# Performance work log

Hardware: AMD Instinct MI355X
Metric: run time of the kernel (lower is better)

Reference implementation:

```python
import jax, jax.numpy as jnp
import numpy as np

V, D, H, L, S_MAX = 32000, 1024, 16, 4, 1024
HD = D // H          # head dim = 64
FF = 4 * D           # mlp hidden = 4096
B, S = 2, 1024


def _layernorm(x, w, b, eps=1e-5):
    mu = jnp.mean(x, axis=-1, keepdims=True)
    var = jnp.mean(jnp.square(x - mu), axis=-1, keepdims=True)
    return (x - mu) * jax.lax.rsqrt(var + eps) * w + b


def setup_inputs() -> dict:
    key = jax.random.key(0)
    ks = jax.random.split(key, 16)
    r = lambda k, shape: (jax.random.normal(k, shape, dtype=jnp.float32) * 0.02)
    return {
        "input_ids": jax.random.randint(ks[0], (B, S), 0, V),
        "tok_emb": r(ks[1], (V, D)),
        "pos_emb": r(ks[2], (S_MAX, D)),
        "ln1_w": jnp.ones((L, D)), "ln1_b": jnp.zeros((L, D)),
        "ln2_w": jnp.ones((L, D)), "ln2_b": jnp.zeros((L, D)),
        "q_w": r(ks[3], (L, D, D)), "q_b": jnp.zeros((L, D)),
        "k_w": r(ks[4], (L, D, D)), "k_b": jnp.zeros((L, D)),
        "v_w": r(ks[5], (L, D, D)), "v_b": jnp.zeros((L, D)),
        "o_w": r(ks[6], (L, D, D)), "o_b": jnp.zeros((L, D)),
        "fc1_w": r(ks[7], (L, FF, D)), "fc1_b": jnp.zeros((L, FF)),
        "fc2_w": r(ks[8], (L, D, FF)), "fc2_b": jnp.zeros((L, D)),
        "lnf_w": jnp.ones((D,)), "lnf_b": jnp.zeros((D,)),
        "head_w": r(ks[9], (V, D)),
    }


def reference(input_ids, tok_emb, pos_emb, ln1_w, ln1_b, ln2_w, ln2_b,
              q_w, q_b, k_w, k_b, v_w, v_b, o_w, o_b,
              fc1_w, fc1_b, fc2_w, fc2_b, lnf_w, lnf_b, head_w):
    b, s = input_ids.shape
    x = tok_emb[input_ids] + pos_emb[:s][None, :, :]          # [B,S,D]
    causal = jnp.tril(jnp.ones((s, s), dtype=bool))           # [S,S]
    scale = 1.0 / np.sqrt(HD)
    for i in range(L):
        # --- causal MHA block ---
        h = _layernorm(x, ln1_w[i], ln1_b[i])
        q = (h @ q_w[i].T + q_b[i]).reshape(b, s, H, HD)
        k = (h @ k_w[i].T + k_b[i]).reshape(b, s, H, HD)
        v = (h @ v_w[i].T + v_b[i]).reshape(b, s, H, HD)
        scores = jnp.einsum('bqhd,bkhd->bhqk', q, k) * scale  # [B,H,S,S]
        scores = jnp.where(causal[None, None], scores, -jnp.inf)
        attn = jax.nn.softmax(scores, axis=-1)
        y = jnp.einsum('bhqk,bkhd->bqhd', attn, v).reshape(b, s, D)
        x = x + (y @ o_w[i].T + o_b[i])
        # --- GELU MLP block (exact gelu, matching torch F.gelu default) ---
        h = _layernorm(x, ln2_w[i], ln2_b[i])
        h = jax.nn.gelu(h @ fc1_w[i].T + fc1_b[i], approximate=False)
        x = x + (h @ fc2_w[i].T + fc2_b[i])
    x = _layernorm(x, lnf_w, lnf_b)
    logits = x[:, -1, :] @ head_w.T                           # [B,V]
    return logits
```

## Files before the change

### kernel.cpp

```cpp
#include <hip/hip_runtime.h>

#define V_SIZE 32000
#define D_DIM  1024
#define H_HEADS 16
#define L_LAYERS 4
#define HD_DIM 64
#define FF_DIM 4096
#define B_BATCH 2
#define S_SEQ  1024
#define M_ROWS (B_BATCH*S_SEQ)
#define KSPL   2

typedef short  s16x8 __attribute__((ext_vector_type(8)));
typedef unsigned short u16x8 __attribute__((ext_vector_type(8)));
typedef float  f32x4 __attribute__((ext_vector_type(4)));
typedef unsigned short u16;
typedef unsigned int   u32;

__device__ inline u16 f2bf(float f){
    u32 u = __float_as_uint(f);
    return (u16)((u + 0x7FFFu + ((u >> 16) & 1u)) >> 16);
}
__device__ inline float b2f(u32 v){ return __uint_as_float(v << 16); }

__device__ inline float gelu_f(float v){
    float y = 0.7978845608f * (v + 0.044715f*v*v*v);
    y = fmaxf(-15.f, fminf(15.f, y));
    float u = __expf(-2.f*y);
    return v / (1.f + u);
}

__device__ inline char* lds_swz(void* base, int row, int byteoff){
    return (char*)base + row*128 + (byteoff ^ ((row & 7) << 4));
}

__device__ inline void gload16(const u16* g, u16* l){
    __builtin_amdgcn_global_load_lds(
        (const __attribute__((address_space(1))) void*)g,
        (__attribute__((address_space(3))) void*)l, 16, 0, 0);
}

__device__ inline int swz_src_col(int lin){
    int row = lin >> 3, s8 = lin & 7;
    return (s8*8) ^ ((row & 7) << 3);
}

__device__ inline s16x8 cvt8(float4 a, float4 b){
    s16x8 o;
    o[0]=(short)f2bf(a.x); o[1]=(short)f2bf(a.y);
    o[2]=(short)f2bf(a.z); o[3]=(short)f2bf(a.w);
    o[4]=(short)f2bf(b.x); o[5]=(short)f2bf(b.y);
    o[6]=(short)f2bf(b.z); o[7]=(short)f2bf(b.w);
    return o;
}

__global__ __launch_bounds__(256) void cvt_all_k(
    const float* __restrict__ qw, const float* __restrict__ kw,
    const float* __restrict__ vw, const float* __restrict__ ow,
    const float* __restrict__ f1w, const float* __restrict__ f2w,
    u16* __restrict__ w_qkv, u16* __restrict__ w_o,
    u16* __restrict__ w_f1, u16* __restrict__ w_f2)
{
    const long M1 = 1L << 20;
    const int bx = blockIdx.x;
    const float* s; u16* d; long base;
    if (bx < 3072){
        int which = bx >> 10;
        s = (which==0) ? qw : ((which==1) ? kw : vw);
        base = (long)(bx & 1023) * 4096;
        long layer = base >> 20, rem = base & (M1 - 1);
        d = w_qkv + layer*3*M1 + which*M1 + rem;
        s += base;
    } else if (bx < 4096){
        base = (long)(bx - 3072) * 4096; s = ow  + base; d = w_o  + base;
    } else if (bx < 8192){
        base = (long)(bx - 4096) * 4096; s = f1w + base; d = w_f1 + base;
    } else {
        base = (long)(bx - 8192) * 4096; s = f2w + base; d = w_f2 + base;
    }
    const int t8 = threadIdx.x * 8;
#pragma unroll
    for (int j = 0; j < 2; j++){
        const float* sp = s + j*2048 + t8;
        float4 v0 = *(const float4*)(sp);
        float4 v1 = *(const float4*)(sp + 4);
        *(s16x8*)(d + j*2048 + t8) = cvt8(v0, v1);
    }
}

__global__ __launch_bounds__(256) void embed_ln_k(
    const int* __restrict__ ids, const float* __restrict__ tok,
    const float* __restrict__ pos, const float* __restrict__ lw,
    const float* __restrict__ lb, float* __restrict__ x, u16* __restrict__ h)
{
    int row = blockIdx.x;
    int id  = ids[row];
    int s   = row & (S_SEQ - 1);
    int t   = threadIdx.x;
    float4 tv = *(const float4*)(tok + (size_t)id * D_DIM + t*4);
    float4 pv = *(const float4*)(pos + (size_t)s  * D_DIM + t*4);
    float4 vv;
    vv.x = tv.x + pv.x; vv.y = tv.y + pv.y; vv.z = tv.z + pv.z; vv.w = tv.w + pv.w;
    *(float4*)(x + (size_t)row * D_DIM + t*4) = vv;
    float sm  = vv.x + vv.y + vv.z + vv.w;
    float ss = vv.x*vv.x + vv.y*vv.y + vv.z*vv.z + vv.w*vv.w;
#pragma unroll
    for (int off = 1; off < 64; off <<= 1){
        sm += __shfl_xor(sm, off);
        ss += __shfl_xor(ss, off);
    }
    __shared__ float red[8];
    const int wid = t >> 6, lane = t & 63;
    if (lane == 0){ red[wid] = sm; red[4 + wid] = ss; }
    __syncthreads();
    sm = red[0] + red[1] + red[2] + red[3];
    ss = red[4] + red[5] + red[6] + red[7];
    float mu   = sm * (1.0f/1024.0f);
    float rstd = rsqrtf(ss * (1.0f/1024.0f) - mu*mu + 1e-5f);
    float4 wv = *(const float4*)(lw + t*4);
    float4 bv = *(const float4*)(lb + t*4);
    uint2 pk;
    pk.x = (u32)f2bf((vv.x-mu)*rstd*wv.x + bv.x) | ((u32)f2bf((vv.y-mu)*rstd*wv.y + bv.y) << 16);
    pk.y = (u32)f2bf((vv.z-mu)*rstd*wv.z + bv.z) | ((u32)f2bf((vv.w-mu)*rstd*wv.w + bv.w) << 16);
    *(uint2*)(h + (size_t)row * D_DIM + t*4) = pk;
}

__global__ __launch_bounds__(256) void reduce_ln_k(
    const u16* __restrict__ part, const float* __restrict__ bias,
    float* __restrict__ x,
    const float* __restrict__ lw, const float* __restrict__ lb,
    u16* __restrict__ h)
{
    const int row = blockIdx.x, t = threadIdx.x;
    const size_t off = (size_t)row * D_DIM + t*4;
    float4 a = *(float4*)(x + off);
    float4 bv = *(const float4*)(bias + t*4);
    a.x += bv.x; a.y += bv.y; a.z += bv.z; a.w += bv.w;
#pragma unroll
    for (int si = 0; si < KSPL; si++){
        uint2 pv = *(const uint2*)(part + (size_t)si * M_ROWS * D_DIM + off);
        a.x += b2f(pv.x & 0xffffu); a.y += b2f(pv.x >> 16);
        a.z += b2f(pv.y & 0xffffu); a.w += b2f(pv.y >> 16);
    }
    *(float4*)(x + off) = a;
    float sm = a.x + a.y + a.z + a.w;
    float ss = a.x*a.x + a.y*a.y + a.z*a.z + a.w*a.w;
#pragma unroll
    for (int o2 = 1; o2 < 64; o2 <<= 1){
        sm += __shfl_xor(sm, o2);
        ss += __shfl_xor(ss, o2);
    }
    __shared__ float red[8];
    const int wid = t >> 6, lane = t & 63;
    if (lane == 0){ red[wid] = sm; red[4 + wid] = ss; }
    __syncthreads();
    sm = red[0] + red[1] + red[2] + red[3];
    ss = red[4] + red[5] + red[6] + red[7];
    float mu   = sm * (1.0f/1024.0f);
    float rstd = rsqrtf(ss * (1.0f/1024.0f) - mu*mu + 1e-5f);
    float4 wv = *(const float4*)(lw + t*4);
    float4 lbv = *(const float4*)(lb + t*4);
    uint2 pk;
    pk.x = (u32)f2bf((a.x-mu)*rstd*wv.x + lbv.x) | ((u32)f2bf((a.y-mu)*rstd*wv.y + lbv.y) << 16);
    pk.y = (u32)f2bf((a.z-mu)*rstd*wv.z + lbv.z) | ((u32)f2bf((a.w-mu)*rstd*wv.w + lbv.w) << 16);
    *(uint2*)(h + (size_t)row * D_DIM + t*4) = pk;
}

__global__ __launch_bounds__(256) void gemm_fc1_k(
    const u16* __restrict__ A, const u16* __restrict__ Bw,
    const float* __restrict__ b0, u16* __restrict__ outB, int Ndim, int Kdim)
{
    const int nx = gridDim.x, ny = gridDim.y;
    const int nwg = nx*ny;
    int orig = blockIdx.y*nx + blockIdx.x;
    int wg = (orig & 7)*(nwg >> 3) + (orig >> 3);
    const int bm = wg % nx;
    const int bn = wg / nx;

    const int nk = Kdim >> 6;

    __shared__ __align__(16) u16 As[2][128*64];
    __shared__ __align__(16) u16 Bs[2][128*64];

    const int t = threadIdx.x;
    const int wid = t >> 6, lane = t & 63, lr = lane & 15, lg = lane >> 4;
    const int wr = wid >> 1, wc = wid & 1;

    f32x4 acc[4][4];
#pragma unroll
    for (int m=0;m<4;m++)
#pragma unroll
        for (int n=0;n<4;n++) acc[m][n] = (f32x4){0.f,0.f,0.f,0.f};

    const u16* Abase = A  + (size_t)(bm*128)*Kdim;
    const u16* Bbase = Bw + (size_t)(bn*128)*Kdim;

    auto stage = [&](int koff, int buf){
#pragma unroll
        for (int i=0;i<4;i++){
            int lin = i*256 + t;
            int row = lin >> 3;
            int sc  = swz_src_col(lin);
            gload16(Abase + (size_t)row*Kdim + koff + sc, &As[buf][lin*8]);
        }
#pragma unroll
        for (int i=0;i<4;i++){
            int lin = i*256 + t;
            int row = lin >> 3;
            int sc  = swz_src_col(lin);
            gload16(Bbase + (size_t)row*Kdim + koff + sc, &Bs[buf][lin*8]);
        }
    };

    stage(0, 0);
    __syncthreads();
    int cb = 0;
    for (int ki = 0; ki < nk; ki++){
        if (ki+1 < nk) stage((ki+1)*64, cb^1);
#pragma unroll
        for (int kk=0;kk<2;kk++){
            s16x8 a[4], b[4];
#pragma unroll
            for (int m=0;m<4;m++)
                a[m] = *(s16x8*)lds_swz(As[cb], wr*64 + m*16 + lr, kk*64 + lg*16);
#pragma unroll
            for (int n=0;n<4;n++)
                b[n] = *(s16x8*)lds_swz(Bs[cb], wc*64 + n*16 + lr, kk*64 + lg*16);
#pragma unroll
            for (int m=0;m<4;m++)
#pragma unroll
                for (int n=0;n<4;n++)
                    acc[m][n] = __builtin_amdgcn_mfma_f32_16x16x32_bf16(a[m], b[n], acc[m][n], 0, 0, 0);
        }
        __syncthreads();
        cb ^= 1;
    }

#pragma unroll
    for (int n=0;n<4;n++){
        int col = bn*128 + wc*64 + n*16 + lr;
        float bvv = b0[col];
#pragma unroll
        for (int m=0;m<4;m++){
            int row0 = bm*128 + wr*64 + m*16 + lg*4;
#pragma unroll
            for (int j=0;j<4;j++){
                int row = row0 + j;
                float val = gelu_f(acc[m][n][j] + bvv);
                outB[(size_t)row * Ndim + col] = f2bf(val);
            }
        }
    }
}

template<int QSEG>
__global__ __launch_bounds__(256) void gemm64o_k(
    const u16* __restrict__ A, const u16* __restrict__ Bw,
    const float* __restrict__ b0, const float* __restrict__ b1, const float* __restrict__ b2,
    u16* __restrict__ outB, int Ndim, int Kdim)
{
    const int nx = gridDim.x, ny = gridDim.y;
    const int nwg = nx*ny;
    int orig = blockIdx.y*nx + blockIdx.x;
    int wg = (orig & 7)*(nwg >> 3) + (orig >> 3);
    const int bm = wg % nx;
    const int bn = wg / nx;
    const int nk = Kdim >> 6;

    __shared__ __align__(16) u16 As[2][64*64];
    __shared__ __align__(16) u16 Bs[2][128*64];

    const int t = threadIdx.x;
    const int wid = t >> 6, lane = t & 63, lr = lane & 15, lg = lane >> 4;
    const int wr = wid >> 1, wc = wid & 1;

    f32x4 acc[2][4];
#pragma unroll
    for (int m=0;m<2;m++)
#pragma unroll
        for (int n=0;n<4;n++) acc[m][n] = (f32x4){0.f,0.f,0.f,0.f};

    const u16* Abase = A  + (size_t)(bm*64)*Kdim;
    const u16* Bbase = Bw + (size_t)(bn*128)*Kdim;

    auto stage = [&](int koff, int buf){
#pragma unroll
        for (int i=0;i<2;i++){
            int lin = i*256 + t;
            int row = lin >> 3;
            int sc  = swz_src_col(lin);
            gload16(Abase + (size_t)row*Kdim + koff + sc, &As[buf][lin*8]);
        }
#pragma unroll
        for (int i=0;i<4;i++){
            int lin = i*256 + t;
            int row = lin >> 3;
            int sc  = swz_src_col(lin);
            gload16(Bbase + (size_t)row*Kdim + koff + sc, &Bs[buf][lin*8]);
        }
    };

    stage(0, 0);
    __syncthreads();
    int cb = 0;
    for (int ki = 0; ki < nk; ki++){
        if (ki+1 < nk) stage((ki+1)*64, cb^1);
#pragma unroll
        for (int kk=0;kk<2;kk++){
            s16x8 a[2], b[4];
#pragma unroll
            for (int m=0;m<2;m++)
                a[m] = *(s16x8*)lds_swz(As[cb], wr*32 + m*16 + lr, kk*64 + lg*16);
#pragma unroll
            for (int n=0;n<4;n++)
                b[n] = *(s16x8*)lds_swz(Bs[cb], wc*64 + n*16 + lr, kk*64 + lg*16);
#pragma unroll
            for (int m=0;m<2;m++)
#pragma unroll
                for (int n=0;n<4;n++)
                    acc[m][n] = __builtin_amdgcn_mfma_f32_16x16x32_bf16(a[m], b[n], acc[m][n], 0, 0, 0);
        }
        __syncthreads();
        cb ^= 1;
    }

#pragma unroll
    for (int n=0;n<4;n++){
        int col = bn*128 + wc*64 + n*16 + lr;
        int which = col >> 10;
        const float* bp = (which==0) ? b0 : ((which==1) ? b1 : b2);
        float bvv = bp[col & 1023];
        float scl = (which == QSEG) ? 0.125f : 1.0f;
#pragma unroll
        for (int m=0;m<2;m++){
            int row0 = bm*64 + wr*32 + m*16 + lg*4;
#pragma unroll
            for (int j=0;j<4;j++){
                int row = row0 + j;
                float val = (acc[m][n][j] + bvv) * scl;
                outB[(size_t)row * Ndim + col] = f2bf(val);
            }
        }
    }
}

__global__ __launch_bounds__(256) void gemm64_k(
    const u16* __restrict__ A, const u16* __restrict__ Bw,
    u16* __restrict__ outP, int Ndim, int Kdim, int kper)
{
    const int nx = gridDim.x, ny = gridDim.y;
    const int nwg = nx*ny*gridDim.z;
    int orig = (blockIdx.z*ny + blockIdx.y)*nx + blockIdx.x;
    int wg = (orig & 7)*(nwg >> 3) + (orig >> 3);
    const int bm = wg % nx; wg /= nx;
    const int bn = wg % ny;
    const int z  = wg / ny;
    const int kbeg = z * kper;
    const int nk = kper >> 6;

    __shared__ __align__(16) u16 As[2][64*64];
    __shared__ __align__(16) u16 Bs[2][128*64];

    const int t = threadIdx.x;
    const int wid = t >> 6, lane = t & 63, lr = lane & 15, lg = lane >> 4;
    const int wr = wid >> 1, wc = wid & 1;

    f32x4 acc[2][4];
#pragma unroll
    for (int m=0;m<2;m++)
#pragma unroll
        for (int n=0;n<4;n++) acc[m][n] = (f32x4){0.f,0.f,0.f,0.f};

    const u16* Abase = A  + (size_t)(bm*64)*Kdim + kbeg;
    const u16* Bbase = Bw + (size_t)(bn*128)*Kdim + kbeg;

    auto stage = [&](int koff, int buf){
#pragma unroll
        for (int i=0;i<2;i++){
            int lin = i*256 + t;
            int row = lin >> 3;
            int sc  = swz_src_col(lin);
            gload16(Abase + (size_t)row*Kdim + koff + sc, &As[buf][lin*8]);
        }
#pragma unroll
        for (int i=0;i<4;i++){
            int lin = i*256 + t;
            int row = lin >> 3;
            int sc  = swz_src_col(lin);
            gload16(Bbase + (size_t)row*Kdim + koff + sc, &Bs[buf][lin*8]);
        }
    };

    stage(0, 0);
    __syncthreads();
    int cb = 0;
    for (int ki = 0; ki < nk; ki++){
        if (ki+1 < nk) stage((ki+1)*64, cb^1);
#pragma unroll
        for (int kk=0;kk<2;kk++){
            s16x8 a[2], b[4];
#pragma unroll
            for (int m=0;m<2;m++)
                a[m] = *(s16x8*)lds_swz(As[cb], wr*32 + m*16 + lr, kk*64 + lg*16);
#pragma unroll
            for (int n=0;n<4;n++)
                b[n] = *(s16x8*)lds_swz(Bs[cb], wc*64 + n*16 + lr, kk*64 + lg*16);
#pragma unroll
            for (int m=0;m<2;m++)
#pragma unroll
                for (int n=0;n<4;n++)
                    acc[m][n] = __builtin_amdgcn_mfma_f32_16x16x32_bf16(a[m], b[n], acc[m][n], 0, 0, 0);
        }
        __syncthreads();
        cb ^= 1;
    }

#pragma unroll
    for (int n=0;n<4;n++){
        int col = bn*128 + wc*64 + n*16 + lr;
#pragma unroll
        for (int m=0;m<2;m++){
            int row0 = bm*64 + wr*32 + m*16 + lg*4;
#pragma unroll
            for (int j=0;j<4;j++){
                int row = row0 + j;
                outP[(size_t)z * M_ROWS * Ndim + (size_t)row * Ndim + col] = f2bf(acc[m][n][j]);
            }
        }
    }
}

__global__ __launch_bounds__(256) void attn_k(
    const u16* __restrict__ qkv, u16* __restrict__ y)
{
    const int gx = gridDim.x;
    const int nwg = gx * gridDim.y;
    int orig = blockIdx.y*gx + blockIdx.x;
    int wg = (orig & 7)*(nwg >> 3) + (orig >> 3);
    const int p  = wg % gx;
    const int bh = wg / gx;
    const int b  = bh >> 4, h = bh & 15;

    const int s_lo = p, s_hi = 15 - p;
    const int ntiles = s_hi + 1;

    __shared__ __align__(16) u16 Ks[2][64*64];
    __shared__ __align__(16) u16 VTs[2][64*64];
    __shared__ __align__(16) u16 Ps[4][16*64];

    const int t = threadIdx.x, wid = t >> 6, lane = t & 63, lr = lane & 15, lg = lane >> 4;
    const size_t rowb = (size_t)b * S_SEQ;
    const u16* qp = qkv + h*HD_DIM;
    const u16* kp = qkv + 1024 + h*HD_DIM;
    const u16* vp = qkv + 2048 + h*HD_DIM;

    const int qw_lo = s_lo*64 + wid*16;
    const int qw_hi = s_hi*64 + wid*16;

    s16x8 aq_lo[2], aq_hi[2];
#pragma unroll
    for (int kc=0;kc<2;kc++){
        aq_lo[kc] = *(const s16x8*)(qp + (rowb + qw_lo + lr) * 3072 + kc*32 + lg*8);
        aq_hi[kc] = *(const s16x8*)(qp + (rowb + qw_hi + lr) * 3072 + kc*32 + lg*8);
    }

    f32x4 o_lo[4], o_hi[4];
#pragma unroll
    for (int n=0;n<4;n++){ o_lo[n] = (f32x4){0.f,0.f,0.f,0.f}; o_hi[n] = (f32x4){0.f,0.f,0.f,0.f}; }
    float l_lo[4] = {0.f,0.f,0.f,0.f}, l_hi[4] = {0.f,0.f,0.f,0.f};

    const int kpr = t >> 3, dsl = t & 7;
    u16x8 vr0, vr1;

    auto issueK = [&](int kt, int buf){
#pragma unroll
        for (int i=0;i<2;i++){
            int lin = i*256 + t;
            int row = lin >> 3;
            int sc  = swz_src_col(lin);
            gload16(kp + (rowb + kt*64 + row)*3072 + sc, &Ks[buf][lin*8]);
        }
    };
    auto loadV = [&](int kt){
        vr0 = *(const u16x8*)(vp + (rowb + kt*64 + 2*kpr    )*3072 + dsl*8);
        vr1 = *(const u16x8*)(vp + (rowb + kt*64 + 2*kpr + 1)*3072 + dsl*8);
    };
    auto writeVT = [&](int buf){
#pragma unroll
        for (int j=0;j<8;j++){
            u32 pk = (u32)vr0[j] | ((u32)vr1[j] << 16);
            *(u32*)lds_swz(VTs[buf], dsl*8 + j, kpr*4) = pk;
        }
    };

    auto doStrip = [&](const s16x8* aq, f32x4* o, float* lsum, int qwS, int kt, bool diag, int cb){
        f32x4 sf[4];
#pragma unroll
        for (int n=0;n<4;n++) sf[n] = (f32x4){0.f,0.f,0.f,0.f};
        __builtin_amdgcn_s_setprio(1);
#pragma unroll
        for (int kc=0;kc<2;kc++){
#pragma unroll
            for (int n=0;n<4;n++){
                s16x8 bk = *(s16x8*)lds_swz(Ks[cb], n*16 + lr, kc*64 + lg*16);
                sf[n] = __builtin_amdgcn_mfma_f32_16x16x32_bf16(aq[kc], bk, sf[n], 0, 0, 0);
            }
        }
        __builtin_amdgcn_s_setprio(0);
        float rs[4] = {0.f,0.f,0.f,0.f};
#pragma unroll
        for (int n=0;n<4;n++){
            int key = kt*64 + n*16 + lr;
#pragma unroll
            for (int j=0;j<4;j++){
                float pe = __expf(sf[n][j]);
                if (diag && key > qwS + lg*4 + j) pe = 0.f;
                sf[n][j] = pe; rs[j] += pe;
            }
        }
#pragma unroll
        for (int off=1; off<16; off<<=1){
#pragma unroll
            for (int j=0;j<4;j++) rs[j] += __shfl_xor(rs[j], off);
        }
#pragma unroll
        for (int j=0;j<4;j++) lsum[j] += rs[j];
        u16* Pw = Ps[wid];
#pragma unroll
        for (int n=0;n<4;n++)
#pragma unroll
            for (int j=0;j<4;j++)
                *(u16*)lds_swz(Pw, lg*4 + j, (n*16 + lr)*2) = f2bf(sf[n][j]);
        __builtin_amdgcn_s_setprio(1);
#pragma unroll
        for (int kc=0;kc<2;kc++){
            s16x8 pa = *(s16x8*)lds_swz(Pw, lr, kc*64 + lg*16);
#pragma unroll
            for (int n=0;n<4;n++){
                s16x8 bv = *(s16x8*)lds_swz(VTs[cb], n*16 + lr, kc*64 + lg*16);
                o[n] = __builtin_amdgcn_mfma_f32_16x16x32_bf16(pa, bv, o[n], 0, 0, 0);
            }
        }
        __builtin_amdgcn_s_setprio(0);
    };

    issueK(0, 0); loadV(0); writeVT(0);
    __syncthreads();
    int cb = 0;
    for (int kt = 0; kt < ntiles; kt++){
        const bool more = (kt+1 < ntiles);
        if (more){ issueK(kt+1, cb^1); loadV(kt+1); }

        doStrip(aq_hi, o_hi, l_hi, qw_hi, kt, kt == s_hi, cb);
        if (kt <= s_lo)
            doStrip(aq_lo, o_lo, l_lo, qw_lo, kt, kt == s_lo, cb);

        if (more) writeVT(cb^1);
        __syncthreads();
        cb ^= 1;
    }

    float inv_lo[4], inv_hi[4];
#pragma unroll
    for (int j=0;j<4;j++){ inv_lo[j] = 1.0f / l_lo[j]; inv_hi[j] = 1.0f / l_hi[j]; }
#pragma unroll
    for (int n=0;n<4;n++)
#pragma unroll
        for (int j=0;j<4;j++){
            y[(rowb + qw_hi + lg*4 + j) * D_DIM + h*HD_DIM + n*16 + lr] = f2bf(o_hi[n][j] * inv_hi[j]);
            y[(rowb + qw_lo + lg*4 + j) * D_DIM + h*HD_DIM + n*16 + lr] = f2bf(o_lo[n][j] * inv_lo[j]);
        }
}

__global__ __launch_bounds__(256) void attn_last_k(
    const u16* __restrict__ q2, const u16* __restrict__ kv,
    float* __restrict__ Yp, float* __restrict__ psp)
{
    const int chunk = blockIdx.x;
    const int bh = blockIdx.y;
    const int b = bh >> 4, h = bh & 15;
    const int t = threadIdx.x;
    const size_t rowb = (size_t)b * S_SEQ;
    __shared__ float qs[64];
    __shared__ float ps[256];
    __shared__ float red[4];
    __shared__ float yred[4][64];
    if (t < 64) qs[t] = b2f(q2[b*1024 + h*HD_DIM + t]);
    __syncthreads();
    int k = chunk*256 + t;
    const u16* krow = kv + (rowb + k)*2048 + h*HD_DIM;
    float s = 0.f;
#pragma unroll
    for (int j=0;j<8;j++){
        u16x8 kv8 = *(const u16x8*)(krow + j*8);
#pragma unroll
        for (int e=0;e<8;e++) s += qs[j*8+e] * b2f((u32)(unsigned short)kv8[e]);
    }
    float p = __expf(s);
    ps[t] = p;
    float sp_ = p;
#pragma unroll
    for (int off=1; off<64; off<<=1) sp_ += __shfl_xor(sp_, off);
    if ((t & 63) == 0) red[t>>6] = sp_;
    __syncthreads();
    if (t == 0) psp[chunk*32 + bh] = red[0]+red[1]+red[2]+red[3];
    int d = t & 63, c = t >> 6;
    float acc = 0.f;
    const u16* vbase = kv + (rowb + chunk*256 + c*64)*2048 + 1024 + h*HD_DIM + d;
    for (int kk=0; kk<64; kk++)
        acc += ps[c*64 + kk] * b2f((u32)vbase[(size_t)kk*2048]);
    yred[c][d] = acc;
    __syncthreads();
    if (t < 64)
        Yp[(chunk*32 + bh)*64 + t] = yred[0][t]+yred[1][t]+yred[2][t]+yred[3][t];
}

template<int MODE>
__global__ __launch_bounds__(256) void rowpair_k(
    const u16* __restrict__ A0, const u16* __restrict__ A1,
    const float* __restrict__ Yp, const float* __restrict__ psp,
    const float* __restrict__ x2in,
    const float* __restrict__ lw, const float* __restrict__ lb,
    const u16* __restrict__ W, const float* __restrict__ bias,
    const float* __restrict__ xresid,
    float* __restrict__ outF, u16* __restrict__ outB,
    int Ndim, int Kdim)
{
    __shared__ u16 As16[2][1024];
    __shared__ float red[8];
    const int t = threadIdx.x, wid = t >> 6, lane = t & 63;

    if (MODE == 0){
        for (int idx = t; idx < 2048; idx += 256){
            int r = idx >> 10, d10 = idx & 1023;
            int bh = r*16 + (d10 >> 6), d = d10 & 63;
            float psum = psp[bh] + psp[32+bh] + psp[64+bh] + psp[96+bh];
            float yv = Yp[bh*64+d] + Yp[(32+bh)*64+d] + Yp[(64+bh)*64+d] + Yp[(96+bh)*64+d];
            As16[r][d10] = f2bf(yv / psum);
        }
        __syncthreads();
    }
    if (MODE == 1){
#pragma unroll
        for (int r = 0; r < 2; r++){
            float4 vv = *(const float4*)(x2in + r*1024 + t*4);
            float sm = vv.x + vv.y + vv.z + vv.w;
            float ss = vv.x*vv.x + vv.y*vv.y + vv.z*vv.z + vv.w*vv.w;
#pragma unroll
            for (int o2 = 1; o2 < 64; o2 <<= 1){
                sm += __shfl_xor(sm, o2);
                ss += __shfl_xor(ss, o2);
            }
            if (lane == 0){ red[wid] = sm; red[4+wid] = ss; }
            __syncthreads();
            sm = red[0]+red[1]+red[2]+red[3];
            ss = red[4]+red[5]+red[6]+red[7];
            float mu = sm * (1.0f/1024.0f);
            float rstd = rsqrtf(ss * (1.0f/1024.0f) - mu*mu + 1e-5f);
            float4 wv  = *(const float4*)(lw + t*4);
            float4 lbv = *(const float4*)(lb + t*4);
            As16[r][t*4+0] = f2bf((vv.x-mu)*rstd*wv.x + lbv.x);
            As16[r][t*4+1] = f2bf((vv.y-mu)*rstd*wv.y + lbv.y);
            As16[r][t*4+2] = f2bf((vv.z-mu)*rstd*wv.z + lbv.z);
            As16[r][t*4+3] = f2bf((vv.w-mu)*rstd*wv.w + lbv.w);
            __syncthreads();
        }
    }

    const u16* pa0 = (MODE==0 || MODE==1) ? (const u16*)As16[0] : A0;
    const u16* pa1 = (MODE==0 || MODE==1) ? (const u16*)As16[1] : A1;

    const int colsPerBlock = Ndim >> 8;
    const int colsPerWave  = colsPerBlock >> 2;
    const int nj = Kdim >> 9;
    for (int cc = 0; cc < colsPerWave; cc++){
        int col = blockIdx.x * colsPerBlock + wid * colsPerWave + cc;
        const u16* wrow = W + (size_t)col * Kdim;
        float s0 = 0.f, s1 = 0.f;
        for (int j = 0; j < nj; j++){
            int k = j*512 + lane*8;
            u16x8 wv = *(const u16x8*)(wrow + k);
            u16x8 a0 = *(const u16x8*)(pa0 + k);
            u16x8 a1 = *(const u16x8*)(pa1 + k);
#pragma unroll
            for (int e=0;e<8;e++){
                float wf = b2f((u32)wv[e]);
                s0 += b2f((u32)a0[e]) * wf;
                s1 += b2f((u32)a1[e]) * wf;
            }
        }
#pragma unroll
        for (int off=1; off<64; off<<=1){
            s0 += __shfl_xor(s0, off);
            s1 += __shfl_xor(s1, off);
        }
        if (lane == 0){
            float bv = bias[col];
            if (MODE == 0){
                outF[col]         = xresid[(size_t)(S_SEQ-1)*D_DIM + col]   + bv + s0;
                outF[D_DIM + col] = xresid[(size_t)(2*S_SEQ-1)*D_DIM + col] + bv + s1;
            } else if (MODE == 1){
                outB[col]         = f2bf(gelu_f(s0 + bv));
                outB[Ndim + col]  = f2bf(gelu_f(s1 + bv));
            } else if (MODE == 2){
                outF[col]         = x2in[col]         + bv + s0;
                outF[D_DIM + col] = x2in[D_DIM + col] + bv + s1;
            } else {
                outB[col]         = f2bf((s0 + bv) * 0.125f);
                outB[Ndim + col]  = f2bf((s1 + bv) * 0.125f);
            }
        }
    }
}

__global__ __launch_bounds__(256) void head_ln_k(
    const float* __restrict__ x3, const float* __restrict__ w, const float* __restrict__ bb,
    const float* __restrict__ hw, float* __restrict__ out)
{
    __shared__ float xs[2*D_DIM];
    __shared__ float red[8];
    int t = threadIdx.x, wid = t >> 6, lane = t & 63;
#pragma unroll
    for (int r = 0; r < 2; r++){
        float4 vv = *(const float4*)(x3 + r*D_DIM + t*4);
        float s  = vv.x + vv.y + vv.z + vv.w;
        float ss = vv.x*vv.x + vv.y*vv.y + vv.z*vv.z + vv.w*vv.w;
#pragma unroll
        for (int off = 1; off < 64; off <<= 1){
            s  += __shfl_xor(s,  off);
            ss += __shfl_xor(ss, off);
        }
        if (lane == 0){ red[wid] = s; red[4+wid] = ss; }
        __syncthreads();
        s  = red[0]+red[1]+red[2]+red[3];
        ss = red[4]+red[5]+red[6]+red[7];
        float mu   = s * (1.0f/1024.0f);
        float rstd = rsqrtf(ss * (1.0f/1024.0f) - mu*mu + 1e-5f);
        float4 wv = *(const float4*)(w  + t*4);
        float4 bv = *(const float4*)(bb + t*4);
        xs[r*D_DIM + t*4+0] = (vv.x-mu)*rstd*wv.x + bv.x;
        xs[r*D_DIM + t*4+1] = (vv.y-mu)*rstd*wv.y + bv.y;
        xs[r*D_DIM + t*4+2] = (vv.z-mu)*rstd*wv.z + bv.z;
        xs[r*D_DIM + t*4+3] = (vv.w-mu)*rstd*wv.w + bv.w;
        __syncthreads();
    }
    int vrow = blockIdx.x * 4 + wid;
    float s0 = 0.f, s1 = 0.f;
#pragma unroll
    for (int it=0; it<4; it++){
        int j = it*64 + lane;
        float4 w4 = *(const float4*)(hw + (size_t)vrow * D_DIM + j*4);
        float4 x0 = *(const float4*)&xs[j*4];
        float4 x1 = *(const float4*)&xs[D_DIM + j*4];
        s0 += w4.x*x0.x + w4.y*x0.y + w4.z*x0.z + w4.w*x0.w;
        s1 += w4.x*x1.x + w4.y*x1.y + w4.z*x1.z + w4.w*x1.w;
    }
#pragma unroll
    for (int off=1; off<64; off<<=1){
        s0 += __shfl_xor(s0, off);
        s1 += __shfl_xor(s1, off);
    }
    if (lane == 0){
        out[vrow]          = s0;
        out[V_SIZE + vrow] = s1;
    }
}

extern "C" void kernel_launch(void* const* d_in, const int* in_sizes, int n_in,
                              void* d_out, int out_size, void* d_ws, size_t ws_size,
                              hipStream_t stream)
{
    (void)in_sizes; (void)n_in; (void)out_size; (void)ws_size;
    const int*   ids  = (const int*)  d_in[0];
    const float* tok  = (const float*)d_in[1];
    const float* pos  = (const float*)d_in[2];
    const float* ln1w = (const float*)d_in[3];
    const float* ln1b = (const float*)d_in[4];
    const float* ln2w = (const float*)d_in[5];
    const float* ln2b = (const float*)d_in[6];
    const float* qw   = (const float*)d_in[7];
    const float* qbi  = (const float*)d_in[8];
    const float* kw   = (const float*)d_in[9];
    const float* kbi  = (const float*)d_in[10];
    const float* vw   = (const float*)d_in[11];
    const float* vbi  = (const float*)d_in[12];
    const float* ow   = (const float*)d_in[13];
    const float* obi  = (const float*)d_in[14];
    const float* f1w  = (const float*)d_in[15];
    const float* f1b  = (const float*)d_in[16];
    const float* f2w  = (const float*)d_in[17];
    const float* f2b  = (const float*)d_in[18];
    const float* lnfw = (const float*)d_in[19];
    const float* lnfb = (const float*)d_in[20];
    const float* hw   = (const float*)d_in[21];

    const long MD = (long)1024*1024;
    char* p = (char*)d_ws;
    float* x    = (float*)p; p += (size_t)M_ROWS * D_DIM * 4;
    u16* h      = (u16*)p;   p += (size_t)M_ROWS * D_DIM * 2;
    u16* qkvbuf = (u16*)p;   p += (size_t)M_ROWS * 3072 * 2;
    u16* ybuf   = (u16*)p;   p += (size_t)M_ROWS * D_DIM * 2;
    u16* h1     = (u16*)p;   p += (size_t)M_ROWS * FF_DIM * 2;
    u16* part   = (u16*)p;   p += (size_t)KSPL * M_ROWS * D_DIM * 2;
    u16* wbuf   = (u16*)p;   p += (size_t)48 * MD * 2;
    u16*   q2   = (u16*)p;   p += 2 * D_DIM * 2;
    float* x2   = (float*)p; p += 2 * D_DIM * 4;
    float* x3   = (float*)p; p += 2 * D_DIM * 4;
    u16*   g2   = (u16*)p;   p += 2 * FF_DIM * 2;
    float* Yp   = (float*)p; p += 4 * 32 * 64 * 4;
    float* psp  = (float*)p; p += 4 * 32 * 4;
    float* logits = (float*)d_out;

    u16* w_qkv = wbuf;
    u16* w_o   = wbuf + 12*MD;
    u16* w_f1  = wbuf + 16*MD;
    u16* w_f2  = wbuf + 32*MD;

    cvt_all_k<<<dim3(12288), 256, 0, stream>>>(
        qw, kw, vw, ow, f1w, f2w, w_qkv, w_o, w_f1, w_f2);

    embed_ln_k<<<dim3(M_ROWS), 256, 0, stream>>>(ids, tok, pos, ln1w, ln1b, x, h);

    for (int i = 0; i < L_LAYERS - 1; i++){
        gemm64o_k<0><<<dim3(32, 24), 256, 0, stream>>>(
            h, w_qkv + (size_t)i*3*MD,
            qbi + i*D_DIM, kbi + i*D_DIM, vbi + i*D_DIM,
            qkvbuf, 3072, D_DIM);
        attn_k<<<dim3(8, 32), 256, 0, stream>>>(qkvbuf, ybuf);
        gemm64_k<<<dim3(32, 8, KSPL), 256, 0, stream>>>(
            ybuf, w_o + (size_t)i*MD, part, D_DIM, D_DIM, D_DIM/KSPL);
        reduce_ln_k<<<dim3(M_ROWS), 256, 0, stream>>>(
            part, obi + i*D_DIM, x, ln2w + i*D_DIM, ln2b + i*D_DIM, h);
        gemm_fc1_k<<<dim3(16, 32), 256, 0, stream>>>(
            h, w_f1 + (size_t)i*4*MD, f1b + i*FF_DIM, h1, FF_DIM, D_DIM);
        gemm64_k<<<dim3(32, 8, KSPL), 256, 0, stream>>>(
            h1, w_f2 + (size_t)i*4*MD, part, D_DIM, FF_DIM, FF_DIM/KSPL);
        reduce_ln_k<<<dim3(M_ROWS), 256, 0, stream>>>(
            part, f2b + i*D_DIM, x, ln1w + (i+1)*D_DIM, ln1b + (i+1)*D_DIM, h);
    }

    const int L3 = L_LAYERS - 1;
    gemm64o_k<-1><<<dim3(32, 16), 256, 0, stream>>>(
        h, w_qkv + (size_t)L3*3*MD + MD,
        kbi + L3*D_DIM, vbi + L3*D_DIM, vbi + L3*D_DIM,
        qkvbuf, 2048, D_DIM);
    rowpair_k<3><<<dim3(256), 256, 0, stream>>>(
        h + (size_t)(S_SEQ-1)*D_DIM, h + (size_t)(2*S_SEQ-1)*D_DIM,
        nullptr, nullptr, nullptr, nullptr, nullptr,
        w_qkv + (size_t)L3*3*MD, qbi + L3*D_DIM, nullptr,
        nullptr, q2, D_DIM, D_DIM);
    attn_last_k<<<dim3(4, 32), 256, 0, stream>>>(q2, qkvbuf, Yp, psp);
    rowpair_k<0><<<dim3(256), 256, 0, stream>>>(
        nullptr, nullptr, Yp, psp, nullptr, nullptr, nullptr,
        w_o + (size_t)L3*MD, obi + L3*D_DIM, x,
        x2, nullptr, D_DIM, D_DIM);
    rowpair_k<1><<<dim3(256), 256, 0, stream>>>(
        nullptr, nullptr, nullptr, nullptr, x2,
        ln2w + L3*D_DIM, ln2b + L3*D_DIM,
        w_f1 + (size_t)L3*4*MD, f1b + L3*FF_DIM, nullptr,
        nullptr, g2, FF_DIM, D_DIM);
    rowpair_k<2><<<dim3(256), 256, 0, stream>>>(
        g2, g2 + FF_DIM, nullptr, nullptr, x2, nullptr, nullptr,
        w_f2 + (size_t)L3*4*MD, f2b + L3*D_DIM, nullptr,
        x3, nullptr, D_DIM, FF_DIM);
    head_ln_k<<<dim3(V_SIZE/4), 256, 0, stream>>>(x3, lnfw, lnfb, hw, logits);
}
```

Before: 538.9 us.

## Split attention lo/hi query strips across 8 waves in 512-thread blocks

Doubles the attention block to 512 threads so four waves handle the low query strip and four handle the high strip, instead of each wave processing both strips serially. K loads are done by the upper half of threads and V transpose by the lower half. This raises per-block parallelism and halves per-wave register state, but the waves on the low strip sit idle once past their diagonal tile, so work is imbalanced inside the block and barrier waits grow.

```diff
diff --git a/kernel.cpp b/kernel.cpp
--- a/kernel.cpp
+++ b/kernel.cpp
@@ -430,7 +430,7 @@
     }
 }
 
-__global__ __launch_bounds__(256) void attn_k(
+__global__ __launch_bounds__(512) void attn_k(
     const u16* __restrict__ qkv, u16* __restrict__ y)
 {
     const int gx = gridDim.x;
@@ -446,7 +446,7 @@
 
     __shared__ __align__(16) u16 Ks[2][64*64];
     __shared__ __align__(16) u16 VTs[2][64*64];
-    __shared__ __align__(16) u16 Ps[4][16*64];
+    __shared__ __align__(16) u16 Ps[8][16*64];
 
     const int t = threadIdx.x, wid = t >> 6, lane = t & 63, lr = lane & 15, lg = lane >> 4;
     const size_t rowb = (size_t)b * S_SEQ;
@@ -454,46 +454,51 @@
     const u16* kp = qkv + 1024 + h*HD_DIM;
     const u16* vp = qkv + 2048 + h*HD_DIM;
 
-    const int qw_lo = s_lo*64 + wid*16;
-    const int qw_hi = s_hi*64 + wid*16;
-
-    s16x8 aq_lo[2], aq_hi[2];
-#pragma unroll
-    for (int kc=0;kc<2;kc++){
-        aq_lo[kc] = *(const s16x8*)(qp + (rowb + qw_lo + lr) * 3072 + kc*32 + lg*8);
-        aq_hi[kc] = *(const s16x8*)(qp + (rowb + qw_hi + lr) * 3072 + kc*32 + lg*8);
-    }
-
-    f32x4 o_lo[4], o_hi[4];
-#pragma unroll
-    for (int n=0;n<4;n++){ o_lo[n] = (f32x4){0.f,0.f,0.f,0.f}; o_hi[n] = (f32x4){0.f,0.f,0.f,0.f}; }
-    float l_lo[4] = {0.f,0.f,0.f,0.f}, l_hi[4] = {0.f,0.f,0.f,0.f};
+    const int s  = (wid >= 4) ? s_hi : s_lo;
+    const int wq = wid & 3;
+    const int qw = s*64 + wq*16;
+
+    s16x8 aq[2];
+#pragma unroll
+    for (int kc=0;kc<2;kc++)
+        aq[kc] = *(const s16x8*)(qp + (rowb + qw + lr) * 3072 + kc*32 + lg*8);
+
+    f32x4 o[4];
+#pragma unroll
+    for (int n=0;n<4;n++) o[n] = (f32x4){0.f,0.f,0.f,0.f};
+    float lsum[4] = {0.f,0.f,0.f,0.f};
 
     const int kpr = t >> 3, dsl = t & 7;
     u16x8 vr0, vr1;
 
     auto issueK = [&](int kt, int buf){
-#pragma unroll
-        for (int i=0;i<2;i++){
-            int lin = i*256 + t;
-            int row = lin >> 3;
-            int sc  = swz_src_col(lin);
-            gload16(kp + (rowb + kt*64 + row)*3072 + sc, &Ks[buf][lin*8]);
+        if (t >= 256){
+#pragma unroll
+            for (int i=0;i<2;i++){
+                int lin = i*256 + (t - 256);
+                int row = lin >> 3;
+                int sc  = swz_src_col(lin);
+                gload16(kp + (rowb + kt*64 + row)*3072 + sc, &Ks[buf][lin*8]);
+            }
         }
     };
     auto loadV = [&](int kt){
-        vr0 = *(const u16x8*)(vp + (rowb + kt*64 + 2*kpr    )*3072 + dsl*8);
-        vr1 = *(const u16x8*)(vp + (rowb + kt*64 + 2*kpr + 1)*3072 + dsl*8);
+        if (t < 256){
+            vr0 = *(const u16x8*)(vp + (rowb + kt*64 + 2*kpr    )*3072 + dsl*8);
+            vr1 = *(const u16x8*)(vp + (rowb + kt*64 + 2*kpr + 1)*3072 + dsl*8);
+        }
     };
     auto writeVT = [&](int buf){
-#pragma unroll
-        for (int j=0;j<8;j++){
-            u32 pk = (u32)vr0[j] | ((u32)vr1[j] << 16);
-            *(u32*)lds_swz(VTs[buf], dsl*8 + j, kpr*4) = pk;
+        if (t < 256){
+#pragma unroll
+            for (int j=0;j<8;j++){
+                u32 pk = (u32)vr0[j] | ((u32)vr1[j] << 16);
+                *(u32*)lds_swz(VTs[buf], dsl*8 + j, kpr*4) = pk;
+            }
         }
     };
 
-    auto doStrip = [&](const s16x8* aq, f32x4* o, float* lsum, int qwS, int kt, bool diag, int cb){
+    auto doTile = [&](int kt, int cb){
         f32x4 sf[4];
 #pragma unroll
         for (int n=0;n<4;n++) sf[n] = (f32x4){0.f,0.f,0.f,0.f};
@@ -507,6 +512,7 @@
             }
         }
         __builtin_amdgcn_s_setprio(0);
+        const bool diag = (kt == s);
         float rs[4] = {0.f,0.f,0.f,0.f};
 #pragma unroll
         for (int n=0;n<4;n++){
@@ -514,7 +520,7 @@
 #pragma unroll
             for (int j=0;j<4;j++){
                 float pe = __expf(sf[n][j]);
-                if (diag && key > qwS + lg*4 + j) pe = 0.f;
+                if (diag && key > qw + lg*4 + j) pe = 0.f;
                 sf[n][j] = pe; rs[j] += pe;
             }
         }
@@ -551,25 +557,21 @@
         const bool more = (kt+1 < ntiles);
         if (more){ issueK(kt+1, cb^1); loadV(kt+1); }
 
-        doStrip(aq_hi, o_hi, l_hi, qw_hi, kt, kt == s_hi, cb);
-        if (kt <= s_lo)
-            doStrip(aq_lo, o_lo, l_lo, qw_lo, kt, kt == s_lo, cb);
+        if (kt <= s) doTile(kt, cb);
 
         if (more) writeVT(cb^1);
         __syncthreads();
         cb ^= 1;
     }
 
-    float inv_lo[4], inv_hi[4];
-#pragma unroll
-    for (int j=0;j<4;j++){ inv_lo[j] = 1.0f / l_lo[j]; inv_hi[j] = 1.0f / l_hi[j]; }
+    float inv[4];
+#pragma unroll
+    for (int j=0;j<4;j++) inv[j] = 1.0f / lsum[j];
 #pragma unroll
     for (int n=0;n<4;n++)
 #pragma unroll
-        for (int j=0;j<4;j++){
-            y[(rowb + qw_hi + lg*4 + j) * D_DIM + h*HD_DIM + n*16 + lr] = f2bf(o_hi[n][j] * inv_hi[j]);
-            y[(rowb + qw_lo + lg*4 + j) * D_DIM + h*HD_DIM + n*16 + lr] = f2bf(o_lo[n][j] * inv_lo[j]);
-        }
+        for (int j=0;j<4;j++)
+            y[(rowb + qw + lg*4 + j) * D_DIM + h*HD_DIM + n*16 + lr] = f2bf(o[n][j] * inv[j]);
 }
 
 __global__ __launch_bounds__(256) void attn_last_k(
@@ -826,7 +828,7 @@
             h, w_qkv + (size_t)i*3*MD,
             qbi + i*D_DIM, kbi + i*D_DIM, vbi + i*D_DIM,
             qkvbuf, 3072, D_DIM);
-        attn_k<<<dim3(8, 32), 256, 0, stream>>>(qkvbuf, ybuf);
+        attn_k<<<dim3(8, 32), 512, 0, stream>>>(qkvbuf, ybuf);
         gemm64_k<<<dim3(32, 8, KSPL), 256, 0, stream>>>(
             ybuf, w_o + (size_t)i*MD, part, D_DIM, D_DIM, D_DIM/KSPL);
         reduce_ln_k<<<dim3(M_ROWS), 256, 0, stream>>>(
```

Measured after the change: 529.3 us, median of 2. About the same (-1.8%).
